# Optimization experiments

Hardware: AMD Instinct MI355X
Metric: run time of the kernel (lower is better)

## Reference

```python
import jax, jax.numpy as jnp
import numpy as np

SOW_INIT = 1e-10  # sum_of_weights_initial_value
EPS = 1e-8       # torch.nn.CosineSimilarity default eps


def setup_inputs() -> dict:
    key = jax.random.key(0)
    k1, k2, k3 = jax.random.split(key, 3)
    input_image = jax.random.normal(k1, (1, 3, 224, 224), dtype=jnp.float32)
    masks = jax.random.uniform(k2, (1000, 224, 224), dtype=jnp.float32)
    # Linear encoder: flattened image [3*224*224] -> feature dim 128
    W = jax.random.normal(k3, (3, 224, 224, 128), dtype=jnp.float32) * 0.01
    return {"input_image": input_image, "masks": masks, "W": W}


def reference(input_image, masks, W):
    img = input_image[0]  # [3, H, W]
    # Encoder applied to (img * mask): rep_n = sum_chw (img*mask)[c,h,w] * W[c,h,w,f]
    # Precompute A[h,w,f] = sum_c img[c,h,w] * W[c,h,w,f] so masked reps never
    # materialize the [N,3,H,W] masked-image tensor.
    A = jnp.einsum('chw,chwf->hwf', img, W)          # [H, W, F]
    rep0 = jnp.sum(A, axis=(0, 1))                   # unmasked representation [F]
    reps = jnp.einsum('nhw,hwf->nf', masks, A)       # masked representations [N, F]

    # Cosine similarity (dim=1), clamped norms as in torch
    n0 = jnp.maximum(jnp.linalg.norm(rep0), EPS)
    nr = jnp.maximum(jnp.linalg.norm(reps, axis=1), EPS)
    sims = (reps @ rep0) / (nr * n0)                 # [N]

    H, Wd = masks.shape[1], masks.shape[2]
    imp0 = jnp.zeros((H, Wd), dtype=jnp.float32)
    unc0 = jnp.zeros((H, Wd), dtype=jnp.float32)
    sow0 = jnp.full((H, Wd), SOW_INIT, dtype=jnp.float32)

    def step(carry, inp):
        imp, unc, sow = carry
        m, s = inp  # mask [H,W], similarity scalar
        sow = sow + m
        prev = imp
        imp = imp + m * (s - imp) / sow
        unc = unc + (s - imp) * (s - prev) * m
        return (imp, unc, sow), None

    (imp, unc, sow), _ = jax.lax.scan(step, (imp0, unc0, sow0), (masks, sims))
    return jnp.stack([imp, unc, sow])  # [3, H, W]
```

## Files before the change

### kernel.cpp

```cpp
#include <hip/hip_runtime.h>
#include <hip/hip_bf16.h>
#include <stdint.h>

#define HWN 50176
#define NM  1000
#define FD  128
#define NSPLIT 49
#define KSTEPS 32
#define NSCAN 20
#define NPB 50

typedef __attribute__((ext_vector_type(8))) short short8;
typedef __attribute__((ext_vector_type(4))) float f32x4;

__device__ __forceinline__ unsigned short f2bf(float x) {
    union { float f; unsigned u; } v; v.f = x;
    unsigned r = v.u + 0x7FFFu + ((v.u >> 16) & 1u);
    return (unsigned short)(r >> 16);
}

#define AS1(p) ((const __attribute__((address_space(1))) unsigned int*)(p))
#define AS3(p) ((__attribute__((address_space(3))) unsigned int*)(p))

__global__ __launch_bounds__(256) void k_encode(const float* __restrict__ img,
                                                const float* __restrict__ Wt,
                                                unsigned short* __restrict__ Bpack,
                                                float* __restrict__ rep0part)
{
    const int t = threadIdx.x;
    const int f = t & 127;
    const int kt = blockIdx.x * 2 + (t >> 7);
    const int hw0 = kt * 32;
    float vals[32];
    float rsum = 0.f;
#pragma unroll
    for (int e = 0; e < 32; ++e) {
        const int hw = hw0 + e;
        float a = img[hw] * __builtin_nontemporal_load(Wt + (size_t)hw * FD + f);
        a = fmaf(img[HWN + hw],     __builtin_nontemporal_load(Wt + (size_t)(HWN + hw) * FD + f), a);
        a = fmaf(img[2 * HWN + hw], __builtin_nontemporal_load(Wt + (size_t)(2 * HWN + hw) * FD + f), a);
        vals[e] = a;
        rsum += a;
    }
    char* tile = (char*)Bpack + (size_t)kt * 8192;
#pragma unroll
    for (int j = 0; j < 4; ++j) {
        short8 pk;
#pragma unroll
        for (int e = 0; e < 8; ++e) pk[e] = (short)f2bf(vals[j * 8 + e]);
        const int slot = (f * 4 + j) ^ ((f >> 1) & 3);
        *reinterpret_cast<short8*>(tile + (slot << 4)) = pk;
    }
    __shared__ float red[256];
    red[t] = rsum;
    __syncthreads();
    if (t < 128) rep0part[(size_t)blockIdx.x * 128 + f] = red[t] + red[t + 128];
}

__global__ __launch_bounds__(256) void k_rep0red(const float* __restrict__ rep0part,
                                                 float* __restrict__ rep0)
{
    const int f = blockIdx.x;
    float s = 0.f;
    for (int b = threadIdx.x; b < 784; b += 256) s += rep0part[(size_t)b * 128 + f];
    __shared__ float red[256];
    red[threadIdx.x] = s;
    __syncthreads();
    for (int o = 128; o > 0; o >>= 1) {
        if (threadIdx.x < o) red[threadIdx.x] += red[threadIdx.x + o];
        __syncthreads();
    }
    if (threadIdx.x == 0) rep0[f] = red[0];
}

__global__ __launch_bounds__(256, 4) void k_gemm(const float* __restrict__ masks,
                                                 const unsigned short* __restrict__ Bpack,
                                                 float* __restrict__ partial)
{
    __shared__ __align__(16) char Bs[3][8192];

    const int t = threadIdx.x;
    const int wv = t >> 6, lane = t & 63;
    const int lrow = lane & 15, kg = lane >> 4;

    const int bid = blockIdx.x;
    const int swz = (bid & 7) * 98 + (bid >> 3);
    const int split = swz >> 4, mtile = swz & 15;
    const int n0 = mtile * 64;

    int row = n0 + wv * 16 + lrow;
    if (row >= NM) row = NM - 1;
    const float* aSrc = masks + (size_t)row * HWN + split * 1024 + kg * 8;
    const char*  bSrc = (const char*)Bpack + (size_t)split * (KSTEPS * 8192) + t * 16;

    int bo[8];
#pragma unroll
    for (int ft = 0; ft < 8; ++ft) {
        const int f = ft * 16 + lrow;
        bo[ft] = ((f * 4 + kg) ^ ((f >> 1) & 3)) << 4;
    }

    f32x4 acc[8];
#pragma unroll
    for (int i = 0; i < 8; ++i) acc[i] = f32x4{0.f, 0.f, 0.f, 0.f};

    f32x4 aA0, aA1, aB0, aB1, aC0, aC1;

#define STAGE(KS, BUFOFF) do {                                                                     \
        __builtin_amdgcn_global_load_lds(AS1(bSrc + (size_t)(KS) * 8192),        AS3(&Bs[0][0] + (BUFOFF) + ((t & 255) * 16)), 16, 0, 0); \
        __builtin_amdgcn_global_load_lds(AS1(bSrc + (size_t)(KS) * 8192 + 4096), AS3(&Bs[0][0] + (BUFOFF) + 4096 + ((t & 255) * 16)), 16, 0, 0); \
    } while (0)

    __builtin_amdgcn_sched_barrier(0);
    STAGE(0, 0);
    aA0 = *reinterpret_cast<const f32x4*>(aSrc);
    aA1 = *reinterpret_cast<const f32x4*>(aSrc + 4);
    __builtin_amdgcn_sched_barrier(0);
    STAGE(1, 8192);
    aB0 = *reinterpret_cast<const f32x4*>(aSrc + 32);
    aB1 = *reinterpret_cast<const f32x4*>(aSrc + 36);
    __builtin_amdgcn_sched_barrier(0);

    int boff_c = 0;
    for (int ks = 0; ks < KSTEPS; ++ks) {
        const int boff_s = (boff_c + 16384 >= 24576) ? (boff_c + 16384 - 24576) : (boff_c + 16384);
        if (ks + 2 < KSTEPS) {
            __builtin_amdgcn_sched_barrier(0);
            STAGE(ks + 2, boff_s);
            aC0 = *reinterpret_cast<const f32x4*>(aSrc + (ks + 2) * 32);
            aC1 = *reinterpret_cast<const f32x4*>(aSrc + (ks + 2) * 32 + 4);
            __builtin_amdgcn_sched_barrier(0);
            asm volatile("s_waitcnt vmcnt(8)" ::: "memory");
        } else if (ks == KSTEPS - 2) {
            asm volatile("s_waitcnt vmcnt(4)" ::: "memory");
        } else {
            asm volatile("s_waitcnt vmcnt(0)" ::: "memory");
        }
        __builtin_amdgcn_s_barrier();
        __builtin_amdgcn_sched_barrier(0);

        const char* B = &Bs[0][0] + boff_c;
        short8 bfv[8];
#pragma unroll
        for (int ft = 0; ft < 8; ++ft)
            bfv[ft] = *reinterpret_cast<const short8*>(B + bo[ft]);

        union { short8 s; __hip_bfloat162 h[4]; } apk;
        apk.h[0] = __float22bfloat162_rn(float2{aA0[0], aA0[1]});
        apk.h[1] = __float22bfloat162_rn(float2{aA0[2], aA0[3]});
        apk.h[2] = __float22bfloat162_rn(float2{aA1[0], aA1[1]});
        apk.h[3] = __float22bfloat162_rn(float2{aA1[2], aA1[3]});

        asm volatile("s_waitcnt lgkmcnt(0)" ::: "memory");
        __builtin_amdgcn_sched_barrier(0);
        __builtin_amdgcn_s_setprio(1);
#pragma unroll
        for (int ft = 0; ft < 8; ++ft)
            acc[ft] = __builtin_amdgcn_mfma_f32_16x16x32_bf16(apk.s, bfv[ft], acc[ft], 0, 0, 0);
        __builtin_amdgcn_s_setprio(0);
        __builtin_amdgcn_sched_barrier(0);
        if (ks + 1 < KSTEPS) {
            __builtin_amdgcn_s_barrier();
            __builtin_amdgcn_sched_barrier(0);
        }
        aA0 = aB0; aA1 = aB1; aB0 = aC0; aB1 = aC1;
        boff_c = (boff_c + 8192 >= 24576) ? 0 : (boff_c + 8192);
    }
#undef STAGE

    const int crow = n0 + wv * 16 + (kg << 2);
    float* pb = partial + ((size_t)split * 1024 + crow) * FD + lrow;
#pragma unroll
    for (int ft = 0; ft < 8; ++ft)
#pragma unroll
        for (int rr = 0; rr < 4; ++rr)
            __builtin_nontemporal_store(acc[ft][rr], pb + (size_t)rr * FD + ft * 16);
}

__global__ __launch_bounds__(128) void k_sims(const float* __restrict__ partial,
                                              const float* __restrict__ rep0,
                                              float* __restrict__ sims)
{
    const int n = blockIdx.x;
    const int f = threadIdx.x;
    float rsum = 0.f;
    for (int s = 0; s < NSPLIT; ++s)
        rsum += __builtin_nontemporal_load(partial + ((size_t)s * 1024 + n) * FD + f);
    const float r0 = rep0[f];
    __shared__ float red0[128], red1[128], red2[128];
    red0[f] = rsum * r0;
    red1[f] = rsum * rsum;
    red2[f] = r0 * r0;
    __syncthreads();
    for (int o = 64; o > 0; o >>= 1) {
        if (f < o) {
            red0[f] += red0[f + o];
            red1[f] += red1[f + o];
            red2[f] += red2[f + o];
        }
        __syncthreads();
    }
    if (f == 0) {
        const float nr = fmaxf(sqrtf(red1[0]), 1e-8f);
        const float nz = fmaxf(sqrtf(red2[0]), 1e-8f);
        sims[n] = red0[0] / (nr * nz);
    }
}

__global__ __launch_bounds__(256) void k_colsums(const float* __restrict__ masks,
                                                 const float* __restrict__ sims,
                                                 float* __restrict__ Spart)
{
    __shared__ float s1v[NPB], s2v[NPB];
    const int t = threadIdx.x;
    const int split = blockIdx.y;
    if (t < NPB) {
        const float s = sims[split * NPB + t];
        s1v[t] = s;
        s2v[t] = s * s;
    }
    __syncthreads();
    const int pix = (blockIdx.x * 256 + t) * 4;
    const float* mp = masks + (size_t)split * NPB * HWN + pix;
    f32x4 s0 = {0.f,0.f,0.f,0.f}, s1 = s0, s2 = s0;
#pragma unroll 5
    for (int i = 0; i < NPB; ++i) {
        const f32x4 m = *reinterpret_cast<const f32x4*>(mp + (size_t)i * HWN);
        const float a = s1v[i], b = s2v[i];
        s0 += m;
#pragma unroll
        for (int e = 0; e < 4; ++e) {
            s1[e] = fmaf(m[e], a, s1[e]);
            s2[e] = fmaf(m[e], b, s2[e]);
        }
    }
    float* sp = Spart + (size_t)split * 3 * HWN + pix;
    __builtin_nontemporal_store(s0, reinterpret_cast<f32x4*>(sp));
    __builtin_nontemporal_store(s1, reinterpret_cast<f32x4*>(sp + HWN));
    __builtin_nontemporal_store(s2, reinterpret_cast<f32x4*>(sp + 2 * HWN));
}

__global__ __launch_bounds__(256) void k_final(const float* __restrict__ Spart,
                                               float* __restrict__ out)
{
    const int pix = (blockIdx.x * 256 + threadIdx.x) * 4;
    f32x4 s0 = {0.f,0.f,0.f,0.f}, s1 = s0, s2 = s0;
#pragma unroll 4
    for (int sp = 0; sp < NSCAN; ++sp) {
        const float* p = Spart + (size_t)sp * 3 * HWN + pix;
        s0 += __builtin_nontemporal_load(reinterpret_cast<const f32x4*>(p));
        s1 += __builtin_nontemporal_load(reinterpret_cast<const f32x4*>(p + HWN));
        s2 += __builtin_nontemporal_load(reinterpret_cast<const f32x4*>(p + 2 * HWN));
    }
    f32x4 imp, unc, sow;
#pragma unroll
    for (int e = 0; e < 4; ++e) {
        sow[e] = 1e-10f + s0[e];
        imp[e] = s1[e] / sow[e];
        unc[e] = fmaf(-imp[e], s1[e], s2[e]);
    }
    *reinterpret_cast<f32x4*>(out + pix) = imp;
    *reinterpret_cast<f32x4*>(out + HWN + pix) = unc;
    *reinterpret_cast<f32x4*>(out + 2 * HWN + pix) = sow;
}

extern "C" void kernel_launch(void* const* d_in, const int* in_sizes, int n_in,
                              void* d_out, int out_size, void* d_ws, size_t ws_size,
                              hipStream_t stream) {
    const float* img   = (const float*)d_in[0];
    const float* masks = (const float*)d_in[1];
    const float* Wt    = (const float*)d_in[2];
    float* out = (float*)d_out;

    char* ws = (char*)d_ws;
    unsigned short* Bpack = (unsigned short*)ws;
    float* partial  = (float*)(ws + 12845056);
    float* rep0part = partial;
    float* rep0     = (float*)(ws + 38535168);
    float* sims     = (float*)(ws + 38535680);
    float* Spart    = (float*)ws;

    hipLaunchKernelGGL(k_encode,  dim3(784), dim3(256), 0, stream, img, Wt, Bpack, rep0part);
    hipLaunchKernelGGL(k_rep0red, dim3(128), dim3(256), 0, stream, rep0part, rep0);
    hipLaunchKernelGGL(k_gemm,    dim3(784), dim3(256), 0, stream, masks, Bpack, partial);
    hipLaunchKernelGGL(k_sims,    dim3(NM), dim3(128), 0, stream, partial, rep0, sims);
    hipLaunchKernelGGL(k_colsums, dim3(49, NSCAN), dim3(256), 0, stream, masks, sims, Spart);
    hipLaunchKernelGGL(k_final,   dim3(49), dim3(256), 0, stream, Spart, out);
}
```

Baseline: 123.2 us.

## Restructure GEMM pipeline into 4-kstep windows with double-buffered LDS

Replaces the per-kstep triple-buffered pipeline in the mask×A GEMM with 8 windows of 4 k-steps each. Each window is double-buffered in 64KB of LDS, and the mask loads for a window are issued as a batch. This cuts the number of block-wide barriers and waitcnt points by 4x and puts more memory requests in flight per wave. In exchange, LDS per block grows from 24KB to 64KB and the launch bound drops to 2 blocks per CU, which reduces occupancy and the latency hiding that comes from having many blocks resident.

```diff
diff --git a/kernel.cpp b/kernel.cpp
--- a/kernel.cpp
+++ b/kernel.cpp
@@ -7,6 +7,7 @@
 #define FD  128
 #define NSPLIT 49
 #define KSTEPS 32
+#define NWIN 8
 #define NSCAN 20
 #define NPB 50
 
@@ -73,11 +74,11 @@
     if (threadIdx.x == 0) rep0[f] = red[0];
 }
 
-__global__ __launch_bounds__(256, 4) void k_gemm(const float* __restrict__ masks,
+__global__ __launch_bounds__(256, 2) void k_gemm(const float* __restrict__ masks,
                                                  const unsigned short* __restrict__ Bpack,
                                                  float* __restrict__ partial)
 {
-    __shared__ __align__(16) char Bs[3][8192];
+    __shared__ __align__(16) char Bs[2][32768];
 
     const int t = threadIdx.x;
     const int wv = t >> 6, lane = t & 63;
@@ -104,69 +105,79 @@
 #pragma unroll
     for (int i = 0; i < 8; ++i) acc[i] = f32x4{0.f, 0.f, 0.f, 0.f};
 
-    f32x4 aA0, aA1, aB0, aB1, aC0, aC1;
-
-#define STAGE(KS, BUFOFF) do {                                                                     \
-        __builtin_amdgcn_global_load_lds(AS1(bSrc + (size_t)(KS) * 8192),        AS3(&Bs[0][0] + (BUFOFF) + ((t & 255) * 16)), 16, 0, 0); \
-        __builtin_amdgcn_global_load_lds(AS1(bSrc + (size_t)(KS) * 8192 + 4096), AS3(&Bs[0][0] + (BUFOFF) + 4096 + ((t & 255) * 16)), 16, 0, 0); \
+    f32x4 awin[2][8];
+
+#define STAGE_W(W, P) do {                                                                   \
+        _Pragma("unroll")                                                                    \
+        for (int s4 = 0; s4 < 4; ++s4) {                                                     \
+            awin[P][2 * s4]     = *reinterpret_cast<const f32x4*>(aSrc + (W) * 128 + s4 * 32);     \
+            awin[P][2 * s4 + 1] = *reinterpret_cast<const f32x4*>(aSrc + (W) * 128 + s4 * 32 + 4); \
+        }                                                                                    \
+        _Pragma("unroll")                                                                    \
+        for (int s4 = 0; s4 < 4; ++s4) {                                                     \
+            __builtin_amdgcn_global_load_lds(AS1(bSrc + (size_t)((W) * 4 + s4) * 8192),          \
+                                             AS3(&Bs[P][0] + s4 * 8192 + t * 16), 16, 0, 0);      \
+            __builtin_amdgcn_global_load_lds(AS1(bSrc + (size_t)((W) * 4 + s4) * 8192 + 4096),   \
+                                             AS3(&Bs[P][0] + s4 * 8192 + 4096 + t * 16), 16, 0, 0); \
+        }                                                                                    \
     } while (0)
 
     __builtin_amdgcn_sched_barrier(0);
-    STAGE(0, 0);
-    aA0 = *reinterpret_cast<const f32x4*>(aSrc);
-    aA1 = *reinterpret_cast<const f32x4*>(aSrc + 4);
+    STAGE_W(0, 0);
     __builtin_amdgcn_sched_barrier(0);
-    STAGE(1, 8192);
-    aB0 = *reinterpret_cast<const f32x4*>(aSrc + 32);
-    aB1 = *reinterpret_cast<const f32x4*>(aSrc + 36);
+    STAGE_W(1, 1);
     __builtin_amdgcn_sched_barrier(0);
-
-    int boff_c = 0;
-    for (int ks = 0; ks < KSTEPS; ++ks) {
-        const int boff_s = (boff_c + 16384 >= 24576) ? (boff_c + 16384 - 24576) : (boff_c + 16384);
-        if (ks + 2 < KSTEPS) {
+    asm volatile("s_waitcnt vmcnt(16)" ::: "memory");
+    __builtin_amdgcn_s_barrier();
+    __builtin_amdgcn_sched_barrier(0);
+
+#pragma unroll
+    for (int w = 0; w < NWIN; ++w) {
+        const int P = w & 1;
+#pragma unroll
+        for (int s = 0; s < 4; ++s) {
+            const char* Bb = &Bs[0][0] + P * 32768 + s * 8192;
+            short8 bfv[8];
+#pragma unroll
+            for (int ft = 0; ft < 8; ++ft)
+                bfv[ft] = *reinterpret_cast<const short8*>(Bb + bo[ft]);
+
+            union { short8 sh; __hip_bfloat162 h[4]; } apk;
+            const f32x4 a0 = awin[P][2 * s];
+            const f32x4 a1 = awin[P][2 * s + 1];
+            apk.h[0] = __float22bfloat162_rn(float2{a0[0], a0[1]});
+            apk.h[1] = __float22bfloat162_rn(float2{a0[2], a0[3]});
+            apk.h[2] = __float22bfloat162_rn(float2{a1[0], a1[1]});
+            apk.h[3] = __float22bfloat162_rn(float2{a1[2], a1[3]});
+
+            asm volatile("s_waitcnt lgkmcnt(0)" ::: "memory");
             __builtin_amdgcn_sched_barrier(0);
-            STAGE(ks + 2, boff_s);
-            aC0 = *reinterpret_cast<const f32x4*>(aSrc + (ks + 2) * 32);
-            aC1 = *reinterpret_cast<const f32x4*>(aSrc + (ks + 2) * 32 + 4);
+            __builtin_amdgcn_s_setprio(1);
+#pragma unroll
+            for (int ft = 0; ft < 8; ++ft)
+                acc[ft] = __builtin_amdgcn_mfma_f32_16x16x32_bf16(apk.sh, bfv[ft], acc[ft], 0, 0, 0);
+            __builtin_amdgcn_s_setprio(0);
             __builtin_amdgcn_sched_barrier(0);
-            asm volatile("s_waitcnt vmcnt(8)" ::: "memory");
-        } else if (ks == KSTEPS - 2) {
-            asm volatile("s_waitcnt vmcnt(4)" ::: "memory");
+        }
+        if (w == NWIN - 1) break;
+        __builtin_amdgcn_s_barrier();
+        __builtin_amdgcn_sched_barrier(0);
+        if (w + 2 < NWIN) {
+            if (w + 2 == 2) STAGE_W(2, 0);
+            if (w + 2 == 3) STAGE_W(3, 1);
+            if (w + 2 == 4) STAGE_W(4, 0);
+            if (w + 2 == 5) STAGE_W(5, 1);
+            if (w + 2 == 6) STAGE_W(6, 0);
+            if (w + 2 == 7) STAGE_W(7, 1);
+            __builtin_amdgcn_sched_barrier(0);
+            asm volatile("s_waitcnt vmcnt(16)" ::: "memory");
         } else {
             asm volatile("s_waitcnt vmcnt(0)" ::: "memory");
         }
         __builtin_amdgcn_s_barrier();
         __builtin_amdgcn_sched_barrier(0);
-
-        const char* B = &Bs[0][0] + boff_c;
-        short8 bfv[8];
-#pragma unroll
-        for (int ft = 0; ft < 8; ++ft)
-            bfv[ft] = *reinterpret_cast<const short8*>(B + bo[ft]);
-
-        union { short8 s; __hip_bfloat162 h[4]; } apk;
-        apk.h[0] = __float22bfloat162_rn(float2{aA0[0], aA0[1]});
-        apk.h[1] = __float22bfloat162_rn(float2{aA0[2], aA0[3]});
-        apk.h[2] = __float22bfloat162_rn(float2{aA1[0], aA1[1]});
-        apk.h[3] = __float22bfloat162_rn(float2{aA1[2], aA1[3]});
-
-        asm volatile("s_waitcnt lgkmcnt(0)" ::: "memory");
-        __builtin_amdgcn_sched_barrier(0);
-        __builtin_amdgcn_s_setprio(1);
-#pragma unroll
-        for (int ft = 0; ft < 8; ++ft)
-            acc[ft] = __builtin_amdgcn_mfma_f32_16x16x32_bf16(apk.s, bfv[ft], acc[ft], 0, 0, 0);
-        __builtin_amdgcn_s_setprio(0);
-        __builtin_amdgcn_sched_barrier(0);
-        if (ks + 1 < KSTEPS) {
-            __builtin_amdgcn_s_barrier();
-            __builtin_amdgcn_sched_barrier(0);
-        }
-        aA0 = aB0; aA1 = aB1; aB0 = aC0; aB1 = aC1;
-        boff_c = (boff_c + 8192 >= 24576) ? 0 : (boff_c + 8192);
-    }
-#undef STAGE
+    }
+#undef STAGE_W
 
     const int crow = n0 + wv * 16 + (kg << 2);
     float* pb = partial + ((size_t)split * 1024 + crow) * FD + lrow;
```

Result: slower. 127.5 us (+3.5%).

## Preload bf16 mask tile into LDS and split GEMM into 32-row tiles

Applied to the files above, without the earlier changes.

The GEMM kernel now loads its whole 32x1024 mask slice up front, converts it to bf16 and stores it swizzled in LDS, instead of streaming A from global memory in a triple-buffered pipeline. Each block now covers 32 rows, with waves split across row tiles and feature halves, so the grid doubles to 1568 blocks and B uses double buffering. The aim is better memory-level parallelism for the mask stream and a simpler inner loop. In exchange, 80KB of LDS per block lowers occupancy, and the A load is no longer overlapped with MFMA work inside each block. Each B tile is also now fetched by twice as many blocks.

```diff
diff --git a/kernel.cpp b/kernel.cpp
--- a/kernel.cpp
+++ b/kernel.cpp
@@ -73,105 +73,115 @@
     if (threadIdx.x == 0) rep0[f] = red[0];
 }
 
-__global__ __launch_bounds__(256, 4) void k_gemm(const float* __restrict__ masks,
+__global__ __launch_bounds__(256, 2) void k_gemm(const float* __restrict__ masks,
                                                  const unsigned short* __restrict__ Bpack,
                                                  float* __restrict__ partial)
 {
-    __shared__ __align__(16) char Bs[3][8192];
+    __shared__ __align__(16) char Alds[65536];
+    __shared__ __align__(16) char Blds[2][8192];
 
     const int t = threadIdx.x;
-    const int wv = t >> 6, lane = t & 63;
-    const int lrow = lane & 15, kg = lane >> 4;
+    const int w = t >> 6, l = t & 63;
+    const int lrow = l & 15, kg = l >> 4;
 
     const int bid = blockIdx.x;
-    const int swz = (bid & 7) * 98 + (bid >> 3);
-    const int split = swz >> 4, mtile = swz & 15;
-    const int n0 = mtile * 64;
-
-    int row = n0 + wv * 16 + lrow;
-    if (row >= NM) row = NM - 1;
-    const float* aSrc = masks + (size_t)row * HWN + split * 1024 + kg * 8;
-    const char*  bSrc = (const char*)Bpack + (size_t)split * (KSTEPS * 8192) + t * 16;
-
-    int bo[8];
-#pragma unroll
-    for (int ft = 0; ft < 8; ++ft) {
-        const int f = ft * 16 + lrow;
+    const int swz = (bid & 7) * 196 + (bid >> 3);
+    const int split = swz >> 5, mtile = swz & 31;
+    const int n0 = mtile * 32;
+
+    {
+        const int rbase = w * 8;
+#pragma unroll
+        for (int i = 0; i < 8; ++i) {
+            const int row = rbase + i;
+            int grow = n0 + row; if (grow >= NM) grow = NM - 1;
+            const float* src = masks + (size_t)grow * HWN + split * 1024 + l * 4;
+            f32x4 v0 = *reinterpret_cast<const f32x4*>(src);
+            f32x4 v1 = *reinterpret_cast<const f32x4*>(src + 256);
+            f32x4 v2 = *reinterpret_cast<const f32x4*>(src + 512);
+            f32x4 v3 = *reinterpret_cast<const f32x4*>(src + 768);
+            char* rb = Alds + row * 2048 + (l & 1) * 8;
+            const int cb = (l >> 1);
+            union { __hip_bfloat162 h[2]; uint2 u; } p0, p1, p2, p3;
+            p0.h[0] = __float22bfloat162_rn(float2{v0[0], v0[1]});
+            p0.h[1] = __float22bfloat162_rn(float2{v0[2], v0[3]});
+            p1.h[0] = __float22bfloat162_rn(float2{v1[0], v1[1]});
+            p1.h[1] = __float22bfloat162_rn(float2{v1[2], v1[3]});
+            p2.h[0] = __float22bfloat162_rn(float2{v2[0], v2[1]});
+            p2.h[1] = __float22bfloat162_rn(float2{v2[2], v2[3]});
+            p3.h[0] = __float22bfloat162_rn(float2{v3[0], v3[1]});
+            p3.h[1] = __float22bfloat162_rn(float2{v3[2], v3[3]});
+            *reinterpret_cast<uint2*>(rb + (((0 * 32 + cb) ^ (row & 7)) << 4)) = p0.u;
+            *reinterpret_cast<uint2*>(rb + (((1 * 32 + cb) ^ (row & 7)) << 4)) = p1.u;
+            *reinterpret_cast<uint2*>(rb + (((2 * 32 + cb) ^ (row & 7)) << 4)) = p2.u;
+            *reinterpret_cast<uint2*>(rb + (((3 * 32 + cb) ^ (row & 7)) << 4)) = p3.u;
+        }
+    }
+    __syncthreads();
+
+    const int rt = w & 1, fh = w >> 1;
+    const int arow = rt * 16 + lrow;
+    const char* abase = Alds + arow * 2048;
+    const int axor = arow & 7;
+    int bo[4];
+#pragma unroll
+    for (int ft = 0; ft < 4; ++ft) {
+        const int f = fh * 64 + ft * 16 + lrow;
         bo[ft] = ((f * 4 + kg) ^ ((f >> 1) & 3)) << 4;
     }
-
-    f32x4 acc[8];
-#pragma unroll
-    for (int i = 0; i < 8; ++i) acc[i] = f32x4{0.f, 0.f, 0.f, 0.f};
-
-    f32x4 aA0, aA1, aB0, aB1, aC0, aC1;
-
-#define STAGE(KS, BUFOFF) do {                                                                     \
-        __builtin_amdgcn_global_load_lds(AS1(bSrc + (size_t)(KS) * 8192),        AS3(&Bs[0][0] + (BUFOFF) + ((t & 255) * 16)), 16, 0, 0); \
-        __builtin_amdgcn_global_load_lds(AS1(bSrc + (size_t)(KS) * 8192 + 4096), AS3(&Bs[0][0] + (BUFOFF) + 4096 + ((t & 255) * 16)), 16, 0, 0); \
+    const char* bSrc = (const char*)Bpack + (size_t)split * (KSTEPS * 8192) + t * 16;
+
+    f32x4 acc[4];
+#pragma unroll
+    for (int i = 0; i < 4; ++i) acc[i] = f32x4{0.f, 0.f, 0.f, 0.f};
+
+#define STAGE_B(KS, P) do {                                                                        \
+        __builtin_amdgcn_global_load_lds(AS1(bSrc + (size_t)(KS) * 8192),        AS3(&Blds[P][0] + t * 16), 16, 0, 0);        \
+        __builtin_amdgcn_global_load_lds(AS1(bSrc + (size_t)(KS) * 8192 + 4096), AS3(&Blds[P][0] + 4096 + t * 16), 16, 0, 0); \
     } while (0)
 
     __builtin_amdgcn_sched_barrier(0);
-    STAGE(0, 0);
-    aA0 = *reinterpret_cast<const f32x4*>(aSrc);
-    aA1 = *reinterpret_cast<const f32x4*>(aSrc + 4);
+    STAGE_B(0, 0);
     __builtin_amdgcn_sched_barrier(0);
-    STAGE(1, 8192);
-    aB0 = *reinterpret_cast<const f32x4*>(aSrc + 32);
-    aB1 = *reinterpret_cast<const f32x4*>(aSrc + 36);
-    __builtin_amdgcn_sched_barrier(0);
-
-    int boff_c = 0;
+
     for (int ks = 0; ks < KSTEPS; ++ks) {
-        const int boff_s = (boff_c + 16384 >= 24576) ? (boff_c + 16384 - 24576) : (boff_c + 16384);
-        if (ks + 2 < KSTEPS) {
+        const int cur = ks & 1;
+        if (ks + 1 < KSTEPS) {
+            STAGE_B(ks + 1, cur ^ 1);
             __builtin_amdgcn_sched_barrier(0);
-            STAGE(ks + 2, boff_s);
-            aC0 = *reinterpret_cast<const f32x4*>(aSrc + (ks + 2) * 32);
-            aC1 = *reinterpret_cast<const f32x4*>(aSrc + (ks + 2) * 32 + 4);
-            __builtin_amdgcn_sched_barrier(0);
-            asm volatile("s_waitcnt vmcnt(8)" ::: "memory");
-        } else if (ks == KSTEPS - 2) {
-            asm volatile("s_waitcnt vmcnt(4)" ::: "memory");
+            asm volatile("s_waitcnt vmcnt(2)" ::: "memory");
         } else {
             asm volatile("s_waitcnt vmcnt(0)" ::: "memory");
         }
         __builtin_amdgcn_s_barrier();
         __builtin_amdgcn_sched_barrier(0);
 
-        const char* B = &Bs[0][0] + boff_c;
-        short8 bfv[8];
-#pragma unroll
-        for (int ft = 0; ft < 8; ++ft)
-            bfv[ft] = *reinterpret_cast<const short8*>(B + bo[ft]);
-
-        union { short8 s; __hip_bfloat162 h[4]; } apk;
-        apk.h[0] = __float22bfloat162_rn(float2{aA0[0], aA0[1]});
-        apk.h[1] = __float22bfloat162_rn(float2{aA0[2], aA0[3]});
-        apk.h[2] = __float22bfloat162_rn(float2{aA1[0], aA1[1]});
-        apk.h[3] = __float22bfloat162_rn(float2{aA1[2], aA1[3]});
+        const short8 av = *reinterpret_cast<const short8*>(abase + (((ks * 4 + kg) ^ axor) << 4));
+        const char* B = &Blds[cur][0];
+        short8 bv[4];
+#pragma unroll
+        for (int ft = 0; ft < 4; ++ft)
+            bv[ft] = *reinterpret_cast<const short8*>(B + bo[ft]);
 
         asm volatile("s_waitcnt lgkmcnt(0)" ::: "memory");
         __builtin_amdgcn_sched_barrier(0);
         __builtin_amdgcn_s_setprio(1);
 #pragma unroll
-        for (int ft = 0; ft < 8; ++ft)
-            acc[ft] = __builtin_amdgcn_mfma_f32_16x16x32_bf16(apk.s, bfv[ft], acc[ft], 0, 0, 0);
+        for (int ft = 0; ft < 4; ++ft)
+            acc[ft] = __builtin_amdgcn_mfma_f32_16x16x32_bf16(av, bv[ft], acc[ft], 0, 0, 0);
         __builtin_amdgcn_s_setprio(0);
         __builtin_amdgcn_sched_barrier(0);
         if (ks + 1 < KSTEPS) {
             __builtin_amdgcn_s_barrier();
             __builtin_amdgcn_sched_barrier(0);
         }
-        aA0 = aB0; aA1 = aB1; aB0 = aC0; aB1 = aC1;
-        boff_c = (boff_c + 8192 >= 24576) ? 0 : (boff_c + 8192);
-    }
-#undef STAGE
-
-    const int crow = n0 + wv * 16 + (kg << 2);
-    float* pb = partial + ((size_t)split * 1024 + crow) * FD + lrow;
-#pragma unroll
-    for (int ft = 0; ft < 8; ++ft)
+    }
+#undef STAGE_B
+
+    const int crow = n0 + rt * 16 + (kg << 2);
+    float* pb = partial + ((size_t)split * 1024 + crow) * FD + fh * 64 + lrow;
+#pragma unroll
+    for (int ft = 0; ft < 4; ++ft)
 #pragma unroll
         for (int rr = 0; rr < 4; ++rr)
             __builtin_nontemporal_store(acc[ft][rr], pb + (size_t)rr * FD + ft * 16);
@@ -282,7 +292,7 @@
 
     hipLaunchKernelGGL(k_encode,  dim3(784), dim3(256), 0, stream, img, Wt, Bpack, rep0part);
     hipLaunchKernelGGL(k_rep0red, dim3(128), dim3(256), 0, stream, rep0part, rep0);
-    hipLaunchKernelGGL(k_gemm,    dim3(784), dim3(256), 0, stream, masks, Bpack, partial);
+    hipLaunchKernelGGL(k_gemm,    dim3(1568), dim3(256), 0, stream, masks, Bpack, partial);
     hipLaunchKernelGGL(k_sims,    dim3(NM), dim3(128), 0, stream, partial, rep0, sims);
     hipLaunchKernelGGL(k_colsums, dim3(49, NSCAN), dim3(256), 0, stream, masks, sims, Spart);
     hipLaunchKernelGGL(k_final,   dim3(49), dim3(256), 0, stream, Spart, out);
```

After: 156.8 us. +27.3%, slower.

## Stage mask tiles through LDS with async loads and larger B chunks

Applied to the files above, without the earlier changes.

The GEMM kernel now streams the fp32 mask tiles into swizzled LDS using global_load_lds, double-buffered across two 32-row sub-tiles. B is staged in 64KB chunks covering 8 k-steps at a time, in place of the earlier 3-stage ring of 8KB buffers. Each wave now computes a 16x64 output quarter for two row sub-tiles, and the occupancy hint drops to one block per CU because LDS use reaches about 128KB. The aim is fewer barriers per k-step and better coalesced mask reads, at the cost of occupancy and latency hiding.

```diff
diff --git a/kernel.cpp b/kernel.cpp
--- a/kernel.cpp
+++ b/kernel.cpp
@@ -6,7 +6,6 @@
 #define NM  1000
 #define FD  128
 #define NSPLIT 49
-#define KSTEPS 32
 #define NSCAN 20
 #define NPB 50
 
@@ -73,108 +72,121 @@
     if (threadIdx.x == 0) rep0[f] = red[0];
 }
 
-__global__ __launch_bounds__(256, 4) void k_gemm(const float* __restrict__ masks,
+__global__ __launch_bounds__(256, 1) void k_gemm(const float* __restrict__ masks,
                                                  const unsigned short* __restrict__ Bpack,
                                                  float* __restrict__ partial)
 {
-    __shared__ __align__(16) char Bs[3][8192];
+    __shared__ __align__(16) char Alds[2][32768];
+    __shared__ __align__(16) char Blds[65536];
 
     const int t = threadIdx.x;
-    const int wv = t >> 6, lane = t & 63;
+    const int w = t >> 6, lane = t & 63;
     const int lrow = lane & 15, kg = lane >> 4;
 
     const int bid = blockIdx.x;
     const int swz = (bid & 7) * 98 + (bid >> 3);
-    const int split = swz >> 4, mtile = swz & 15;
-    const int n0 = mtile * 64;
-
-    int row = n0 + wv * 16 + lrow;
-    if (row >= NM) row = NM - 1;
-    const float* aSrc = masks + (size_t)row * HWN + split * 1024 + kg * 8;
-    const char*  bSrc = (const char*)Bpack + (size_t)split * (KSTEPS * 8192) + t * 16;
-
-    int bo[8];
-#pragma unroll
-    for (int ft = 0; ft < 8; ++ft) {
-        const int f = ft * 16 + lrow;
+    const int win = swz >> 4, rg = swz & 15;
+
+    const int kbase = win * 1024;
+
+#define A_STAGE(SP, MT, BUF) do {                                                         \
+        _Pragma("unroll")                                                                 \
+        for (int i = 0; i < 8; ++i) {                                                     \
+            const int rl = i * 4 + w;                                                     \
+            int grow = rg * 64 + (MT) * 32 + rl; if (grow >= NM) grow = NM - 1;           \
+            const float* src = masks + (size_t)grow * HWN + kbase + (SP) * 256            \
+                               + (((lane * 16) ^ ((rl & 7) << 4)) >> 2);                  \
+            __builtin_amdgcn_global_load_lds(AS1(src),                                    \
+                AS3(&Alds[BUF][0] + rl * 1024 + lane * 16), 16, 0, 0);                    \
+        }                                                                                 \
+    } while (0)
+
+#define B_STAGE(SP) do {                                                                  \
+        const char* bsrc = (const char*)Bpack + ((size_t)win * 32 + (SP) * 8) * 8192;     \
+        _Pragma("unroll")                                                                 \
+        for (int j = 0; j < 16; ++j)                                                      \
+            __builtin_amdgcn_global_load_lds(AS1(bsrc + j * 4096 + t * 16),               \
+                AS3(&Blds[0] + j * 4096 + t * 16), 16, 0, 0);                             \
+    } while (0)
+
+    const int rt = w & 1, fh = w >> 1;
+    const int r = rt * 16 + lrow;
+    const int swr = (r & 7) << 4;
+    int bo[4];
+#pragma unroll
+    for (int ft = 0; ft < 4; ++ft) {
+        const int f = fh * 64 + ft * 16 + lrow;
         bo[ft] = ((f * 4 + kg) ^ ((f >> 1) & 3)) << 4;
     }
 
-    f32x4 acc[8];
-#pragma unroll
-    for (int i = 0; i < 8; ++i) acc[i] = f32x4{0.f, 0.f, 0.f, 0.f};
-
-    f32x4 aA0, aA1, aB0, aB1, aC0, aC1;
-
-#define STAGE(KS, BUFOFF) do {                                                                     \
-        __builtin_amdgcn_global_load_lds(AS1(bSrc + (size_t)(KS) * 8192),        AS3(&Bs[0][0] + (BUFOFF) + ((t & 255) * 16)), 16, 0, 0); \
-        __builtin_amdgcn_global_load_lds(AS1(bSrc + (size_t)(KS) * 8192 + 4096), AS3(&Bs[0][0] + (BUFOFF) + 4096 + ((t & 255) * 16)), 16, 0, 0); \
+    f32x4 acc0[4], acc1[4];
+#pragma unroll
+    for (int i = 0; i < 4; ++i) { acc0[i] = f32x4{0.f,0.f,0.f,0.f}; acc1[i] = acc0[i]; }
+
+#define KLOOP(BUF, ACC) do {                                                              \
+        _Pragma("unroll")                                                                 \
+        for (int ks = 0; ks < 8; ++ks) {                                                  \
+            const int o = ks * 128 + kg * 32;                                             \
+            const f32x4 lo = *reinterpret_cast<const f32x4*>(&Alds[BUF][0] + r * 1024 + (o ^ swr));        \
+            const f32x4 hi = *reinterpret_cast<const f32x4*>(&Alds[BUF][0] + r * 1024 + ((o + 16) ^ swr)); \
+            union { short8 s; __hip_bfloat162 h[4]; } apk;                                \
+            apk.h[0] = __float22bfloat162_rn(float2{lo[0], lo[1]});                       \
+            apk.h[1] = __float22bfloat162_rn(float2{lo[2], lo[3]});                       \
+            apk.h[2] = __float22bfloat162_rn(float2{hi[0], hi[1]});                       \
+            apk.h[3] = __float22bfloat162_rn(float2{hi[2], hi[3]});                       \
+            _Pragma("unroll")                                                             \
+            for (int ft = 0; ft < 4; ++ft) {                                              \
+                const short8 bv = *reinterpret_cast<const short8*>(&Blds[0] + ks * 8192 + bo[ft]); \
+                ACC[ft] = __builtin_amdgcn_mfma_f32_16x16x32_bf16(apk.s, bv, ACC[ft], 0, 0, 0);    \
+            }                                                                             \
+        }                                                                                 \
     } while (0)
 
+    A_STAGE(0, 0, 0);
+    B_STAGE(0);
+    A_STAGE(0, 1, 1);
+    asm volatile("s_waitcnt vmcnt(8)" ::: "memory");
+    __builtin_amdgcn_s_barrier();
     __builtin_amdgcn_sched_barrier(0);
-    STAGE(0, 0);
-    aA0 = *reinterpret_cast<const f32x4*>(aSrc);
-    aA1 = *reinterpret_cast<const f32x4*>(aSrc + 4);
-    __builtin_amdgcn_sched_barrier(0);
-    STAGE(1, 8192);
-    aB0 = *reinterpret_cast<const f32x4*>(aSrc + 32);
-    aB1 = *reinterpret_cast<const f32x4*>(aSrc + 36);
-    __builtin_amdgcn_sched_barrier(0);
-
-    int boff_c = 0;
-    for (int ks = 0; ks < KSTEPS; ++ks) {
-        const int boff_s = (boff_c + 16384 >= 24576) ? (boff_c + 16384 - 24576) : (boff_c + 16384);
-        if (ks + 2 < KSTEPS) {
-            __builtin_amdgcn_sched_barrier(0);
-            STAGE(ks + 2, boff_s);
-            aC0 = *reinterpret_cast<const f32x4*>(aSrc + (ks + 2) * 32);
-            aC1 = *reinterpret_cast<const f32x4*>(aSrc + (ks + 2) * 32 + 4);
-            __builtin_amdgcn_sched_barrier(0);
+
+#pragma unroll
+    for (int p = 0; p < 8; ++p) {
+        const int mt = p & 1, buf = p & 1;
+        if (mt == 0) KLOOP(buf, acc0); else KLOOP(buf, acc1);
+        if (p == 7) break;
+        __builtin_amdgcn_s_barrier();
+        __builtin_amdgcn_sched_barrier(0);
+        const int pn = p + 1;
+        if ((pn & 1) == 0) B_STAGE(pn >> 1);
+        if (pn + 1 <= 7) {
+            const int spn = (pn + 1) >> 1, mtn = (pn + 1) & 1;
+            if (spn == 1 && mtn == 0) A_STAGE(1, 0, 0);
+            if (spn == 1 && mtn == 1) A_STAGE(1, 1, 1);
+            if (spn == 2 && mtn == 0) A_STAGE(2, 0, 0);
+            if (spn == 2 && mtn == 1) A_STAGE(2, 1, 1);
+            if (spn == 3 && mtn == 0) A_STAGE(3, 0, 0);
+            if (spn == 3 && mtn == 1) A_STAGE(3, 1, 1);
             asm volatile("s_waitcnt vmcnt(8)" ::: "memory");
-        } else if (ks == KSTEPS - 2) {
-            asm volatile("s_waitcnt vmcnt(4)" ::: "memory");
         } else {
             asm volatile("s_waitcnt vmcnt(0)" ::: "memory");
         }
         __builtin_amdgcn_s_barrier();
         __builtin_amdgcn_sched_barrier(0);
-
-        const char* B = &Bs[0][0] + boff_c;
-        short8 bfv[8];
-#pragma unroll
-        for (int ft = 0; ft < 8; ++ft)
-            bfv[ft] = *reinterpret_cast<const short8*>(B + bo[ft]);
-
-        union { short8 s; __hip_bfloat162 h[4]; } apk;
-        apk.h[0] = __float22bfloat162_rn(float2{aA0[0], aA0[1]});
-        apk.h[1] = __float22bfloat162_rn(float2{aA0[2], aA0[3]});
-        apk.h[2] = __float22bfloat162_rn(float2{aA1[0], aA1[1]});
-        apk.h[3] = __float22bfloat162_rn(float2{aA1[2], aA1[3]});
-
-        asm volatile("s_waitcnt lgkmcnt(0)" ::: "memory");
-        __builtin_amdgcn_sched_barrier(0);
-        __builtin_amdgcn_s_setprio(1);
-#pragma unroll
-        for (int ft = 0; ft < 8; ++ft)
-            acc[ft] = __builtin_amdgcn_mfma_f32_16x16x32_bf16(apk.s, bfv[ft], acc[ft], 0, 0, 0);
-        __builtin_amdgcn_s_setprio(0);
-        __builtin_amdgcn_sched_barrier(0);
-        if (ks + 1 < KSTEPS) {
-            __builtin_amdgcn_s_barrier();
-            __builtin_amdgcn_sched_barrier(0);
+    }
+#undef KLOOP
+#undef A_STAGE
+#undef B_STAGE
+
+    const int crow = rg * 64 + rt * 16 + (kg << 2);
+    float* pb0 = partial + ((size_t)win * 1024 + crow) * FD + fh * 64 + lrow;
+    float* pb1 = pb0 + 32 * FD;
+#pragma unroll
+    for (int ft = 0; ft < 4; ++ft)
+#pragma unroll
+        for (int rr = 0; rr < 4; ++rr) {
+            __builtin_nontemporal_store(acc0[ft][rr], pb0 + (size_t)rr * FD + ft * 16);
+            __builtin_nontemporal_store(acc1[ft][rr], pb1 + (size_t)rr * FD + ft * 16);
         }
-        aA0 = aB0; aA1 = aB1; aB0 = aC0; aB1 = aC1;
-        boff_c = (boff_c + 8192 >= 24576) ? 0 : (boff_c + 8192);
-    }
-#undef STAGE
-
-    const int crow = n0 + wv * 16 + (kg << 2);
-    float* pb = partial + ((size_t)split * 1024 + crow) * FD + lrow;
-#pragma unroll
-    for (int ft = 0; ft < 8; ++ft)
-#pragma unroll
-        for (int rr = 0; rr < 4; ++rr)
-            __builtin_nontemporal_store(acc[ft][rr], pb + (size_t)rr * FD + ft * 16);
 }
 
 __global__ __launch_bounds__(128) void k_sims(const float* __restrict__ partial,
```

Result: slower. 134.5 us (+9.1%).
